# Kernel optimization log

Hardware: AMD Instinct MI355X
Metric: run time of the kernel (lower is better)

Reference implementation:

```python
import jax, jax.numpy as jnp
import numpy as np

OMEGA = 1.5

def _sine(x, W, b, omega=OMEGA):
    return jnp.sin(omega * (x @ W.T + b))

def setup_inputs() -> dict:
    key = jax.random.key(0)
    ks = jax.random.split(key, 17)
    I = J = K = 384
    mid, R = 256, 100
    s = 0.05  # small init scale, mimics uniform(-1/in, 1/in) style init
    return {
        "A_input": jax.random.normal(ks[0], (I, 1), jnp.float32),
        "B_input": jax.random.normal(ks[1], (J, 1), jnp.float32),
        "C_input": jax.random.normal(ks[2], (K, 1), jnp.float32),
        "A_W1": jax.random.normal(ks[3], (mid, 1), jnp.float32) * s,
        "A_b1": jax.random.normal(ks[4], (mid,), jnp.float32) * s,
        "A_W2": jax.random.normal(ks[5], (R, mid), jnp.float32) * s,
        "A_b2": jax.random.normal(ks[6], (R,), jnp.float32) * s,
        "B_W1": jax.random.normal(ks[7], (mid, 1), jnp.float32) * s,
        "B_b1": jax.random.normal(ks[8], (mid,), jnp.float32) * s,
        "B_W2": jax.random.normal(ks[9], (R, mid), jnp.float32) * s,
        "B_b2": jax.random.normal(ks[10], (R,), jnp.float32) * s,
        "C_W1": jax.random.normal(ks[11], (mid, 1), jnp.float32) * s,
        "C_b1": jax.random.normal(ks[12], (mid,), jnp.float32) * s,
        "C_W2": jax.random.normal(ks[13], (mid, mid), jnp.float32) * s,
        "C_b2": jax.random.normal(ks[14], (mid,), jnp.float32) * s,
        "C_W3": jax.random.normal(ks[15], (R, mid), jnp.float32) * s,
        "C_b3": jax.random.normal(ks[16], (R,), jnp.float32) * s,
    }

def reference(A_input, B_input, C_input,
              A_W1, A_b1, A_W2, A_b2,
              B_W1, B_b1, B_W2, B_b2,
              C_W1, C_b1, C_W2, C_b2, C_W3, C_b3):
    # Factor networks
    A = _sine(A_input, A_W1, A_b1) @ A_W2.T + A_b2                  # [I, R]
    B = _sine(B_input, B_W1, B_b1) @ B_W2.T + B_b2                  # [J, R]
    C = _sine(_sine(C_input, C_W1, C_b1), C_W2, C_b2) @ C_W3.T + C_b3  # [K, R]
    # The frozen core is super-diagonal (core[r,r,r]=1), so the permute/matmul
    # chain reduces exactly to the CP contraction sum_r A[i,r]*B[j,r]*C[k,r].
    return jnp.einsum('ir,jr,kr->ijk', A, B, C)  # [I, J, K]
```

## Files before the change

kernel.cpp:

```cpp
#include <hip/hip_runtime.h>
#include <hip/hip_bf16.h>

#define RR 100
#define MID 256
#define NN 384
#define KP 128

typedef __attribute__((ext_vector_type(8))) __bf16 bf16x8;
typedef __attribute__((ext_vector_type(4))) float floatx4;
typedef unsigned short ushort_t;

#define SW(row, ch) ((((row) << 7)) + ((((ch) ^ ((row) & 15))) << 3))

__device__ __forceinline__ ushort_t f2bf(float f) {
  __hip_bfloat16 h = __float2bfloat16(f);
  return __builtin_bit_cast(ushort_t, h);
}

__global__ __launch_bounds__(256) void factors_kernel(
    const float* __restrict__ xA, const float* __restrict__ xB,
    const float* __restrict__ xC,
    const float* __restrict__ AW1, const float* __restrict__ Ab1,
    const float* __restrict__ AW2, const float* __restrict__ Ab2,
    const float* __restrict__ BW1, const float* __restrict__ Bb1,
    const float* __restrict__ BW2, const float* __restrict__ Bb2,
    const float* __restrict__ CW1, const float* __restrict__ Cb1,
    const float* __restrict__ CW2, const float* __restrict__ Cb2,
    const float* __restrict__ CW3, const float* __restrict__ Cb3,
    float* __restrict__ Af, float* __restrict__ Bf,
    ushort_t* __restrict__ Cbf) {
  __shared__ float h[MID];
  __shared__ float h2[MID];
  const int i = blockIdx.x;
  const int net = blockIdx.y;
  const int t = threadIdx.x;

  const float* x  = (net == 0) ? xA  : (net == 1) ? xB  : xC;
  const float* W1 = (net == 0) ? AW1 : (net == 1) ? BW1 : CW1;
  const float* b1 = (net == 0) ? Ab1 : (net == 1) ? Bb1 : Cb1;

  const float xv = x[i];
  h[t] = sinf(1.5f * (xv * W1[t] + b1[t]));
  __syncthreads();

  const float* hlast = h;
  if (net == 2) {
    float acc = Cb2[t];
    const float* __restrict__ w = &CW2[t * MID];
#pragma unroll 4
    for (int m = 0; m < MID; m += 4) {
      const float4 wv = *(const float4*)&w[m];
      const float4 hv = *(const float4*)&h[m];
      acc += hv.x * wv.x;
      acc += hv.y * wv.y;
      acc += hv.z * wv.z;
      acc += hv.w * wv.w;
    }
    h2[t] = sinf(1.5f * acc);
    __syncthreads();
    hlast = h2;
  }

  const float* W2 = (net == 0) ? AW2 : (net == 1) ? BW2 : CW3;
  const float* b2 = (net == 0) ? Ab2 : (net == 1) ? Bb2 : Cb3;

  if (t < KP) {
    float v = 0.0f;
    if (t < RR) {
      float acc = b2[t];
      const float* __restrict__ w = &W2[t * MID];
#pragma unroll 4
      for (int m = 0; m < MID; m += 4) {
        const float4 wv = *(const float4*)&w[m];
        const float4 hv = *(const float4*)&hlast[m];
        acc += hv.x * wv.x;
        acc += hv.y * wv.y;
        acc += hv.z * wv.z;
        acc += hv.w * wv.w;
      }
      v = acc;
    }
    if (net == 0)      Af[i * KP + t] = v;
    else if (net == 1) Bf[i * KP + t] = v;
    else               Cbf[i * KP + t] = f2bf(v);
  }
}

__global__ __launch_bounds__(256, 3) void cp_mfma(
    const float* __restrict__ Af, const float* __restrict__ Bf,
    const ushort_t* __restrict__ Cbf, float* __restrict__ out) {
  __shared__ ushort_t Wt[128 * KP];

  const int i  = blockIdx.z;
  const int j0 = blockIdx.y * 128;
  const int k0 = blockIdx.x * 128;
  const int t  = threadIdx.x;

  {
    const int jx = t >> 1;
    const int hh = t & 1;
    const float* __restrict__ arow = Af + (size_t)i * KP + hh * 64;
    const float* __restrict__ brow = Bf + (size_t)(j0 + jx) * KP + hh * 64;
#pragma unroll
    for (int c = 0; c < 8; ++c) {
      const float4 a0 = *(const float4*)(arow + c * 8);
      const float4 a1 = *(const float4*)(arow + c * 8 + 4);
      const float4 b0 = *(const float4*)(brow + c * 8);
      const float4 b1 = *(const float4*)(brow + c * 8 + 4);
      uint4 wv;
      wv.x = (unsigned)f2bf(a0.x * b0.x) | ((unsigned)f2bf(a0.y * b0.y) << 16);
      wv.y = (unsigned)f2bf(a0.z * b0.z) | ((unsigned)f2bf(a0.w * b0.w) << 16);
      wv.z = (unsigned)f2bf(a1.x * b1.x) | ((unsigned)f2bf(a1.y * b1.y) << 16);
      wv.w = (unsigned)f2bf(a1.z * b1.z) | ((unsigned)f2bf(a1.w * b1.w) << 16);
      *(uint4*)&Wt[SW(jx, hh * 8 + c)] = wv;
    }
  }
  __syncthreads();

  const int lane = t & 63;
  const int w    = t >> 6;
  const int wj   = (w & 1) * 64;
  const int wk   = (w >> 1) * 64;
  const int m16  = lane & 15;
  const int g    = lane >> 4;

  floatx4 acc[4][4];
#pragma unroll
  for (int kf = 0; kf < 4; ++kf)
#pragma unroll
    for (int jf = 0; jf < 4; ++jf) acc[kf][jf] = (floatx4)0.0f;

#pragma unroll
  for (int ks = 0; ks < 4; ++ks) {
    const int rc = (ks * 4 + g) * 8;

    bf16x8 cf[4];
#pragma unroll
    for (int kf = 0; kf < 4; ++kf)
      cf[kf] = *(const bf16x8*)&Cbf[(size_t)(k0 + wk + kf * 16 + m16) * KP + rc];

    bf16x8 wfr[4];
#pragma unroll
    for (int jf = 0; jf < 4; ++jf)
      wfr[jf] = *(const bf16x8*)&Wt[SW(wj + jf * 16 + m16, ks * 4 + g)];

#pragma unroll
    for (int jf = 0; jf < 4; ++jf)
#pragma unroll
      for (int kf = 0; kf < 4; ++kf)
        acc[kf][jf] = __builtin_amdgcn_mfma_f32_16x16x32_bf16(
            cf[kf], wfr[jf], acc[kf][jf], 0, 0, 0);
  }

  const size_t ibase = (size_t)i * NN * NN;
#pragma unroll
  for (int kf = 0; kf < 4; ++kf) {
    const int k = k0 + wk + kf * 16 + g * 4;
#pragma unroll
    for (int jf = 0; jf < 4; ++jf) {
      const int j = j0 + wj + jf * 16 + m16;
      __builtin_nontemporal_store(
          acc[kf][jf], (floatx4*)&out[ibase + (size_t)j * NN + k]);
    }
  }
}

extern "C" void kernel_launch(void* const* d_in, const int* in_sizes, int n_in,
                              void* d_out, int out_size, void* d_ws, size_t ws_size,
                              hipStream_t stream) {
  const float* A_input = (const float*)d_in[0];
  const float* B_input = (const float*)d_in[1];
  const float* C_input = (const float*)d_in[2];
  const float* A_W1 = (const float*)d_in[3];
  const float* A_b1 = (const float*)d_in[4];
  const float* A_W2 = (const float*)d_in[5];
  const float* A_b2 = (const float*)d_in[6];
  const float* B_W1 = (const float*)d_in[7];
  const float* B_b1 = (const float*)d_in[8];
  const float* B_W2 = (const float*)d_in[9];
  const float* B_b2 = (const float*)d_in[10];
  const float* C_W1 = (const float*)d_in[11];
  const float* C_b1 = (const float*)d_in[12];
  const float* C_W2 = (const float*)d_in[13];
  const float* C_b2 = (const float*)d_in[14];
  const float* C_W3 = (const float*)d_in[15];
  const float* C_b3 = (const float*)d_in[16];

  float* Af = (float*)d_ws;
  float* Bf = Af + NN * KP;
  ushort_t* Cbf = (ushort_t*)(Bf + NN * KP);

  dim3 fgrid(NN, 3);
  factors_kernel<<<fgrid, 256, 0, stream>>>(
      A_input, B_input, C_input,
      A_W1, A_b1, A_W2, A_b2,
      B_W1, B_b1, B_W2, B_b2,
      C_W1, C_b1, C_W2, C_b2, C_W3, C_b3,
      Af, Bf, Cbf);

  dim3 grid(NN / 128, NN / 128, NN);
  cp_mfma<<<grid, 256, 0, stream>>>(Af, Bf, Cbf, (float*)d_out);
}
```

Measured before the change: 338.6 us.

## Precompute A*C product once per block and loop over j tiles

The block now builds the elementwise A[i]*C[k] bf16 tile in shared memory once and reuses it across all three j tiles. B becomes the bf16 operand read from global memory, and the grid shrinks to (k tiles, i), so each block writes three output tiles. This reduces redundant product construction and block launch count. In exchange each block does more serial work, there are fewer blocks in flight, and output stores are now plain stores instead of nontemporal ones.

Result: faster. 312.2 us (-7.8%).

```diff
diff --git a/kernel.cpp b/kernel.cpp
--- a/kernel.cpp
+++ b/kernel.cpp
@@ -27,8 +27,8 @@
     const float* __restrict__ CW1, const float* __restrict__ Cb1,
     const float* __restrict__ CW2, const float* __restrict__ Cb2,
     const float* __restrict__ CW3, const float* __restrict__ Cb3,
-    float* __restrict__ Af, float* __restrict__ Bf,
-    ushort_t* __restrict__ Cbf) {
+    float* __restrict__ Af, ushort_t* __restrict__ Bbf,
+    float* __restrict__ Cf) {
   __shared__ float h[MID];
   __shared__ float h2[MID];
   const int i = blockIdx.x;
@@ -81,38 +81,37 @@
       v = acc;
     }
     if (net == 0)      Af[i * KP + t] = v;
-    else if (net == 1) Bf[i * KP + t] = v;
-    else               Cbf[i * KP + t] = f2bf(v);
+    else if (net == 1) Bbf[i * KP + t] = f2bf(v);
+    else               Cf[i * KP + t] = v;
   }
 }
 
 __global__ __launch_bounds__(256, 3) void cp_mfma(
-    const float* __restrict__ Af, const float* __restrict__ Bf,
-    const ushort_t* __restrict__ Cbf, float* __restrict__ out) {
-  __shared__ ushort_t Wt[128 * KP];
-
-  const int i  = blockIdx.z;
-  const int j0 = blockIdx.y * 128;
+    const float* __restrict__ Af, const ushort_t* __restrict__ Bbf,
+    const float* __restrict__ Cf, float* __restrict__ out) {
+  __shared__ ushort_t ACt[128 * KP];
+
+  const int i  = blockIdx.y;
   const int k0 = blockIdx.x * 128;
   const int t  = threadIdx.x;
 
   {
-    const int jx = t >> 1;
+    const int kx = t >> 1;
     const int hh = t & 1;
     const float* __restrict__ arow = Af + (size_t)i * KP + hh * 64;
-    const float* __restrict__ brow = Bf + (size_t)(j0 + jx) * KP + hh * 64;
+    const float* __restrict__ crow = Cf + (size_t)(k0 + kx) * KP + hh * 64;
 #pragma unroll
     for (int c = 0; c < 8; ++c) {
       const float4 a0 = *(const float4*)(arow + c * 8);
       const float4 a1 = *(const float4*)(arow + c * 8 + 4);
-      const float4 b0 = *(const float4*)(brow + c * 8);
-      const float4 b1 = *(const float4*)(brow + c * 8 + 4);
+      const float4 c0 = *(const float4*)(crow + c * 8);
+      const float4 c1 = *(const float4*)(crow + c * 8 + 4);
       uint4 wv;
-      wv.x = (unsigned)f2bf(a0.x * b0.x) | ((unsigned)f2bf(a0.y * b0.y) << 16);
-      wv.y = (unsigned)f2bf(a0.z * b0.z) | ((unsigned)f2bf(a0.w * b0.w) << 16);
-      wv.z = (unsigned)f2bf(a1.x * b1.x) | ((unsigned)f2bf(a1.y * b1.y) << 16);
-      wv.w = (unsigned)f2bf(a1.z * b1.z) | ((unsigned)f2bf(a1.w * b1.w) << 16);
-      *(uint4*)&Wt[SW(jx, hh * 8 + c)] = wv;
+      wv.x = (unsigned)f2bf(a0.x * c0.x) | ((unsigned)f2bf(a0.y * c0.y) << 16);
+      wv.y = (unsigned)f2bf(a0.z * c0.z) | ((unsigned)f2bf(a0.w * c0.w) << 16);
+      wv.z = (unsigned)f2bf(a1.x * c1.x) | ((unsigned)f2bf(a1.y * c1.y) << 16);
+      wv.w = (unsigned)f2bf(a1.z * c1.z) | ((unsigned)f2bf(a1.w * c1.w) << 16);
+      *(uint4*)&ACt[SW(kx, hh * 8 + c)] = wv;
     }
   }
   __syncthreads();
@@ -124,43 +123,44 @@
   const int m16  = lane & 15;
   const int g    = lane >> 4;
 
-  floatx4 acc[4][4];
-#pragma unroll
-  for (int kf = 0; kf < 4; ++kf)
-#pragma unroll
-    for (int jf = 0; jf < 4; ++jf) acc[kf][jf] = (floatx4)0.0f;
-
-#pragma unroll
-  for (int ks = 0; ks < 4; ++ks) {
-    const int rc = (ks * 4 + g) * 8;
-
-    bf16x8 cf[4];
+  const size_t ibase = (size_t)i * NN * NN;
+
+#pragma unroll 1
+  for (int jt = 0; jt < 3; ++jt) {
+    const int jb = jt * 128 + wj;
+
+    floatx4 acc[4][4];
 #pragma unroll
     for (int kf = 0; kf < 4; ++kf)
-      cf[kf] = *(const bf16x8*)&Cbf[(size_t)(k0 + wk + kf * 16 + m16) * KP + rc];
-
-    bf16x8 wfr[4];
-#pragma unroll
-    for (int jf = 0; jf < 4; ++jf)
-      wfr[jf] = *(const bf16x8*)&Wt[SW(wj + jf * 16 + m16, ks * 4 + g)];
-
-#pragma unroll
-    for (int jf = 0; jf < 4; ++jf)
-#pragma unroll
-      for (int kf = 0; kf < 4; ++kf)
-        acc[kf][jf] = __builtin_amdgcn_mfma_f32_16x16x32_bf16(
-            cf[kf], wfr[jf], acc[kf][jf], 0, 0, 0);
-  }
-
-  const size_t ibase = (size_t)i * NN * NN;
-#pragma unroll
-  for (int kf = 0; kf < 4; ++kf) {
-    const int k = k0 + wk + kf * 16 + g * 4;
-#pragma unroll
-    for (int jf = 0; jf < 4; ++jf) {
-      const int j = j0 + wj + jf * 16 + m16;
-      __builtin_nontemporal_store(
-          acc[kf][jf], (floatx4*)&out[ibase + (size_t)j * NN + k]);
+#pragma unroll
+      for (int jf = 0; jf < 4; ++jf) acc[kf][jf] = (floatx4)0.0f;
+
+#pragma unroll
+    for (int ks = 0; ks < 4; ++ks) {
+      const int rc = (ks * 4 + g) * 8;
+
+      bf16x8 cfr[4], bfr[4];
+#pragma unroll
+      for (int f = 0; f < 4; ++f) {
+        cfr[f] = *(const bf16x8*)&ACt[SW(wk + f * 16 + m16, ks * 4 + g)];
+        bfr[f] = *(const bf16x8*)&Bbf[(size_t)(jb + f * 16 + m16) * KP + rc];
+      }
+#pragma unroll
+      for (int jf = 0; jf < 4; ++jf)
+#pragma unroll
+        for (int kf = 0; kf < 4; ++kf)
+          acc[kf][jf] = __builtin_amdgcn_mfma_f32_16x16x32_bf16(
+              cfr[kf], bfr[jf], acc[kf][jf], 0, 0, 0);
+    }
+
+#pragma unroll
+    for (int kf = 0; kf < 4; ++kf) {
+      const int k = k0 + wk + kf * 16 + g * 4;
+#pragma unroll
+      for (int jf = 0; jf < 4; ++jf) {
+        const int j = jb + jf * 16 + m16;
+        *(floatx4*)&out[ibase + (size_t)j * NN + k] = acc[kf][jf];
+      }
     }
   }
 }
@@ -187,8 +187,8 @@
   const float* C_b3 = (const float*)d_in[16];
 
   float* Af = (float*)d_ws;
-  float* Bf = Af + NN * KP;
-  ushort_t* Cbf = (ushort_t*)(Bf + NN * KP);
+  float* Cf = Af + NN * KP;
+  ushort_t* Bbf = (ushort_t*)(Cf + NN * KP);
 
   dim3 fgrid(NN, 3);
   factors_kernel<<<fgrid, 256, 0, stream>>>(
@@ -196,8 +196,8 @@
       A_W1, A_b1, A_W2, A_b2,
       B_W1, B_b1, B_W2, B_b2,
       C_W1, C_b1, C_W2, C_b2, C_W3, C_b3,
-      Af, Bf, Cbf);
-
-  dim3 grid(NN / 128, NN / 128, NN);
-  cp_mfma<<<grid, 256, 0, stream>>>(Af, Bf, Cbf, (float*)d_out);
-}
+      Af, Bbf, Cf);
+
+  dim3 grid(NN / 128, NN);
+  cp_mfma<<<grid, 256, 0, stream>>>(Af, Bbf, Cf, (float*)d_out);
+}
```
